# Optimization experiments

Measured on AMD Instinct MI355X. Metric: run time of the kernel, lower is better.

The kernel has to match this reference:

```python
import jax, jax.numpy as jnp
import numpy as np

NUM_HEADS = 16
EPS = 1e-15


def setup_inputs() -> dict:
    key = jax.random.key(0)
    k1, k2, k3, k4 = jax.random.split(key, 4)
    B, N, C = 4, 16384, 512
    x = jax.random.normal(k1, (B, N, C), dtype=jnp.float32)
    qkv_weight = jax.random.normal(k2, (3 * C, C), dtype=jnp.float32) * 0.02
    proj_weight = jax.random.normal(k3, (C, C), dtype=jnp.float32) * 0.02
    proj_bias = jax.random.normal(k4, (C,), dtype=jnp.float32) * 0.02
    return {"x": x, "qkv_weight": qkv_weight, "proj_weight": proj_weight, "proj_bias": proj_bias}


def reference(x, qkv_weight, proj_weight, proj_bias):
    B, N, C = x.shape
    H = NUM_HEADS
    D = C // H
    # fused linear + ReLU on q,k (v stays linear, per backward: grad_v has no relu mask)
    qkv = (x @ qkv_weight.T).reshape(B, N, 3, C)
    q = jax.nn.relu(qkv[:, :, 0]).reshape(B, N, H, D)
    k = jax.nn.relu(qkv[:, :, 1]).reshape(B, N, H, D)
    v = qkv[:, :, 2].reshape(B, N, H, D)
    qf = q.astype(jnp.float32)
    kf = k.astype(jnp.float32)
    vf = v.astype(jnp.float32)
    # pad v with a ones column -> normalizer row in vk (pad_vk_mm_fwd)
    v_pad = jnp.concatenate([vf, jnp.ones_like(vf[..., :1])], axis=-1)  # [B,N,H,D+1]
    vk = jnp.einsum('bnhc,bnhd->bhcd', v_pad, kf)  # [B,H,D+1,D] accumulated in fp32
    vk_q = jnp.einsum('bnhd,bhcd->bnhc', qf, vk)  # [B,N,H,D+1]
    # fused division by normalizer (vk_q_mm_divide_fwd)
    proj_input = (vk_q[..., :-1] / (vk_q[..., -1:] + EPS)).astype(x.dtype).reshape(B, N, C)
    return proj_input @ proj_weight.T + proj_bias
```

## Files before the change

kernel.cpp:

```cpp
#include <hip/hip_runtime.h>
#include <stdint.h>

#define NB 4
#define SEQ 16384
#define CH 512
#define NH 16
#define HD 32
#define QKVC 1536
#define MROWS (NB * SEQ)

typedef unsigned short u16;
typedef __attribute__((ext_vector_type(8))) short bf16x8;
typedef __attribute__((ext_vector_type(4))) float f32x4;

__device__ __forceinline__ float bf2f(u16 u) {
  union { unsigned int i; float f; } c; c.i = ((unsigned int)u) << 16; return c.f;
}
__device__ __forceinline__ u16 f2bf(float f) {
  union { float f; unsigned int i; } c; c.f = f;
  return (u16)((c.i + 0x7fffu + ((c.i >> 16) & 1u)) >> 16);
}

__device__ __forceinline__ void async16(const u16* g, u16* l) {
  __builtin_amdgcn_global_load_lds((const __attribute__((address_space(1))) void*)g,
                                   (__attribute__((address_space(3))) void*)l,
                                   16, 0, 0);
}

__global__ void prep_kernel(const float* __restrict__ x,
                            const float* __restrict__ qw,
                            const float* __restrict__ pw,
                            u16* __restrict__ xb,
                            u16* __restrict__ qwb,
                            u16* __restrict__ pwb,
                            float* __restrict__ vk) {
  int gid = blockIdx.x * blockDim.x + threadIdx.x;
  int stride = gridDim.x * blockDim.x;

  const float4* x4 = (const float4*)x;
  ushort4* xb4 = (ushort4*)xb;
  for (int i = gid; i < (MROWS * CH / 4); i += stride) {
    float4 v = x4[i];
    ushort4 o; o.x = f2bf(v.x); o.y = f2bf(v.y); o.z = f2bf(v.z); o.w = f2bf(v.w);
    xb4[i] = o;
  }
  const float4* q4 = (const float4*)qw;
  ushort4* qwb4 = (ushort4*)qwb;
  for (int i = gid; i < (QKVC * CH / 4); i += stride) {
    float4 v = q4[i];
    ushort4 o; o.x = f2bf(v.x); o.y = f2bf(v.y); o.z = f2bf(v.z); o.w = f2bf(v.w);
    qwb4[i] = o;
  }
  const float4* p4 = (const float4*)pw;
  ushort4* pwb4 = (ushort4*)pwb;
  for (int i = gid; i < (CH * CH / 4); i += stride) {
    float4 v = p4[i];
    ushort4 o; o.x = f2bf(v.x); o.y = f2bf(v.y); o.z = f2bf(v.z); o.w = f2bf(v.w);
    pwb4[i] = o;
  }
  float4 z; z.x = 0.f; z.y = 0.f; z.z = 0.f; z.w = 0.f;
  float4* vk4 = (float4*)vk;
  for (int i = gid; i < (NB * NH * 33 * 32 / 4); i += stride) vk4[i] = z;
}

template <int N_DIM, bool RELU_QK, bool FINAL>
__global__ __launch_bounds__(256) void gemm_bt_kernel(
    const u16* __restrict__ A, const u16* __restrict__ Bm,
    void* __restrict__ Out, const float* __restrict__ bias) {
  constexpr int K = 512;
  __shared__ u16 As[128 * 32];
  __shared__ u16 Bs[128 * 32];

  const int tid = threadIdx.x;
  const int lane = tid & 63;
  const int w = tid >> 6;
  const long row0 = (long)blockIdx.y * 128;
  const int col0 = blockIdx.x * 128;

  const int l4r = lane >> 2;
  const int l4c = (lane & 3) * 8;
  const int wr = w >> 1, wc = w & 1;
  const int fr = lane & 15;
  const int koff = (lane >> 4) * 8;

  f32x4 acc[4][4];
#pragma unroll
  for (int m = 0; m < 4; m++)
#pragma unroll
    for (int n = 0; n < 4; n++) {
      f32x4 z = {0.f, 0.f, 0.f, 0.f};
      acc[m][n] = z;
    }

  for (int k0 = 0; k0 < K; k0 += 32) {
#pragma unroll
    for (int i = 0; i < 2; i++) {
      const int r = w * 32 + i * 16;
      async16(A + (row0 + r + l4r) * K + k0 + l4c, &As[r * 32]);
      async16(Bm + (long)(col0 + r + l4r) * K + k0 + l4c, &Bs[r * 32]);
    }
    __syncthreads();
    bf16x8 af[4], bfr[4];
#pragma unroll
    for (int m = 0; m < 4; m++)
      af[m] = *(const bf16x8*)&As[(wr * 64 + m * 16 + fr) * 32 + koff];
#pragma unroll
    for (int n = 0; n < 4; n++)
      bfr[n] = *(const bf16x8*)&Bs[(wc * 64 + n * 16 + fr) * 32 + koff];
#pragma unroll
    for (int m = 0; m < 4; m++)
#pragma unroll
      for (int n = 0; n < 4; n++)
        acc[m][n] = __builtin_amdgcn_mfma_f32_16x16x32_bf16(af[m], bfr[n], acc[m][n], 0, 0, 0);
    __syncthreads();
  }

  const long rbase = row0 + wr * 64;
  const int cbase = col0 + wc * 64;
#pragma unroll
  for (int m = 0; m < 4; m++)
#pragma unroll
    for (int n = 0; n < 4; n++)
#pragma unroll
      for (int j = 0; j < 4; j++) {
        long gr = rbase + m * 16 + (lane >> 4) * 4 + j;
        int gc = cbase + n * 16 + fr;
        float v = acc[m][n][j];
        if constexpr (FINAL) {
          ((float*)Out)[gr * N_DIM + gc] = v + bias[gc];
        } else {
          if (RELU_QK && gc < 1024) v = fmaxf(v, 0.f);
          ((u16*)Out)[gr * N_DIM + gc] = f2bf(v);
        }
      }
}

__global__ __launch_bounds__(256) void vk_kernel(const u16* __restrict__ qkv,
                                                 float* __restrict__ vk) {
  __shared__ u16 tile[4][64 * 64];
  __shared__ float red[1056];

  const int tid = threadIdx.x;
  const int lane = tid & 63;
  const int w = tid >> 6;

  for (int i = tid; i < 1056; i += 256) red[i] = 0.f;
  __syncthreads();

  const int bh = blockIdx.x >> 4;
  const int split = blockIdx.x & 15;
  const int b = bh >> 4, h = bh & 15;

  const int s = lane & 7;
  const int rl = lane >> 3;
  const size_t gbase = (size_t)b * SEQ * QKVC + 512 + (size_t)(s >> 2) * 512 +
                       h * 32 + (s & 3) * 8;

  f32x4 acc[2][2];
  f32x4 accs[2];
#pragma unroll
  for (int tc = 0; tc < 2; tc++) {
    f32x4 z = {0.f, 0.f, 0.f, 0.f};
    accs[tc] = z;
#pragma unroll
    for (int td = 0; td < 2; td++) acc[tc][td] = z;
  }
  bf16x8 ones;
#pragma unroll
  for (int j = 0; j < 8; j++) ones[j] = (short)0x3F80;

  const int m = lane & 15;
  const int g = lane >> 4;
  u16* tw = tile[w];
  const int n0w = split * 1024 + w * 256;

  for (int t = 0; t < 4; ++t) {
    const int nt = n0w + t * 64;
#pragma unroll
    for (int p = 0; p < 8; ++p)
      async16(qkv + gbase + (size_t)(nt + p * 8 + rl) * QKVC, &tw[p * 512]);
    asm volatile("s_waitcnt vmcnt(0)" ::: "memory");
#pragma unroll
    for (int kk = 0; kk < 2; ++kk) {
      bf16x8 av[2], bk[2];
#pragma unroll
      for (int tc = 0; tc < 2; tc++)
#pragma unroll
        for (int j = 0; j < 8; j++)
          av[tc][j] = (short)tw[(kk * 32 + g * 8 + j) * 64 + 32 + tc * 16 + m];
#pragma unroll
      for (int td = 0; td < 2; td++)
#pragma unroll
        for (int j = 0; j < 8; j++)
          bk[td][j] = (short)tw[(kk * 32 + g * 8 + j) * 64 + td * 16 + m];
#pragma unroll
      for (int tc = 0; tc < 2; tc++)
#pragma unroll
        for (int td = 0; td < 2; td++)
          acc[tc][td] = __builtin_amdgcn_mfma_f32_16x16x32_bf16(av[tc], bk[td], acc[tc][td], 0, 0, 0);
#pragma unroll
      for (int td = 0; td < 2; td++)
        accs[td] = __builtin_amdgcn_mfma_f32_16x16x32_bf16(ones, bk[td], accs[td], 0, 0, 0);
    }
  }

#pragma unroll
  for (int tc = 0; tc < 2; tc++)
#pragma unroll
    for (int td = 0; td < 2; td++)
#pragma unroll
      for (int j = 0; j < 4; j++)
        atomicAdd(&red[(tc * 16 + g * 4 + j) * 32 + td * 16 + m], acc[tc][td][j]);
  if (lane < 16) {
#pragma unroll
    for (int td = 0; td < 2; td++)
      atomicAdd(&red[1024 + td * 16 + lane], accs[td][0]);
  }
  __syncthreads();
  float* dst = vk + (size_t)bh * 1056;
  for (int i = tid; i < 1056; i += 256) atomicAdd(&dst[i], red[i]);
}

__global__ __launch_bounds__(256) void vkq_kernel(const u16* __restrict__ qkv,
                                                  const float* __restrict__ vk,
                                                  u16* __restrict__ pi) {
  __shared__ float vkl[8 * 1056];
  __shared__ u16 ob[32 * 256];

  const int tid = threadIdx.x;
  const int chunk = blockIdx.x & 511;
  const int hh = (blockIdx.x >> 9) & 1;
  const int b = blockIdx.x >> 10;
  const int n0 = chunk * 32;

  const float* vg = vk + (size_t)(b * NH + hh * 8) * 1056;
  for (int i = tid; i < 8 * 1056; i += 256) vkl[i] = vg[i];
  __syncthreads();

  const int nl = tid & 31;
  const int hl = tid >> 5;
  const float* vkh = &vkl[hl * 1056];

  const u16* qp = qkv + ((size_t)b * SEQ + n0 + nl) * QKVC + (hh * 8 + hl) * 32;
  float qf[32];
#pragma unroll
  for (int s2 = 0; s2 < 4; ++s2) {
    bf16x8 qv = *(const bf16x8*)(qp + s2 * 8);
#pragma unroll
    for (int j = 0; j < 8; ++j) qf[s2 * 8 + j] = bf2f((u16)qv[j]);
  }

  float num[32];
#pragma unroll
  for (int c = 0; c < 32; ++c) {
    float a = 0.f;
#pragma unroll
    for (int d4 = 0; d4 < 8; ++d4) {
      f32x4 vv = *(const f32x4*)&vkh[c * 32 + d4 * 4];
      a = fmaf(qf[d4 * 4 + 0], vv[0], a);
      a = fmaf(qf[d4 * 4 + 1], vv[1], a);
      a = fmaf(qf[d4 * 4 + 2], vv[2], a);
      a = fmaf(qf[d4 * 4 + 3], vv[3], a);
    }
    num[c] = a;
  }
  float den = 0.f;
#pragma unroll
  for (int d4 = 0; d4 < 8; ++d4) {
    f32x4 vv = *(const f32x4*)&vkh[32 * 32 + d4 * 4];
    den = fmaf(qf[d4 * 4 + 0], vv[0], den);
    den = fmaf(qf[d4 * 4 + 1], vv[1], den);
    den = fmaf(qf[d4 * 4 + 2], vv[2], den);
    den = fmaf(qf[d4 * 4 + 3], vv[3], den);
  }
  const float r = 1.0f / (den + 1e-15f);
#pragma unroll
  for (int c = 0; c < 32; ++c) ob[nl * 256 + hl * 32 + c] = f2bf(num[c] * r);
  __syncthreads();

  u16* pg = pi + ((size_t)b * SEQ + n0) * CH + hh * 256;
  for (int i = tid; i < 1024; i += 256) {
    const int n = i >> 5;
    const int u = i & 31;
    *(bf16x8*)(pg + (size_t)n * CH + u * 8) = *(const bf16x8*)&ob[i * 8];
  }
}

extern "C" void kernel_launch(void* const* d_in, const int* in_sizes, int n_in,
                              void* d_out, int out_size, void* d_ws, size_t ws_size,
                              hipStream_t stream) {
  const float* x = (const float*)d_in[0];
  const float* qw = (const float*)d_in[1];
  const float* pw = (const float*)d_in[2];
  const float* bias = (const float*)d_in[3];

  char* ws = (char*)d_ws;
  u16* qkv = (u16*)(ws);
  u16* xb = (u16*)(ws + 201326592);
  u16* qwb = (u16*)(ws + 268435456);
  u16* pwb = (u16*)(ws + 270008320);
  float* vk = (float*)(ws + 270532608);
  u16* pi = xb;

  prep_kernel<<<2048, 256, 0, stream>>>(x, qw, pw, xb, qwb, pwb, vk);
  gemm_bt_kernel<QKVC, true, false>
      <<<dim3(QKVC / 128, MROWS / 128), 256, 0, stream>>>(xb, qwb, qkv, nullptr);
  vk_kernel<<<NB * NH * 16, 256, 0, stream>>>(qkv, vk);
  vkq_kernel<<<NB * 2 * (SEQ / 32), 256, 0, stream>>>(qkv, vk, pi);
  gemm_bt_kernel<CH, false, true>
      <<<dim3(CH / 128, MROWS / 128), 256, 0, stream>>>(pi, pwb, d_out, bias);
}
```

Measured before the change: 360.8 us.

## Replace GEMM with 256x256-tile 8-wave pipelined kernel using swizzled LDS

Both GEMMs move from a 128x128 tile with 4 waves and a single-buffered K=32 loop to a 256x256 tile with 8 waves. The new loop uses K=64 steps with double-buffered async global-to-LDS loads staged in halves, XOR-swizzled LDS addressing to avoid bank conflicts, and s_setprio around MFMA bursts. A remapped block index groups workgroups for better L2 locality. The goal is more data reuse per load and overlap of memory traffic with MFMA work. In exchange it uses 128KB of LDS and more registers, and its manual waitcnt and barrier scheduling is fragile.

Measured after the change: 319.4 us. 11.5% less time.

```diff
diff --git a/kernel.cpp b/kernel.cpp
--- a/kernel.cpp
+++ b/kernel.cpp
@@ -64,67 +64,161 @@
 }
 
 template <int N_DIM, bool RELU_QK, bool FINAL>
-__global__ __launch_bounds__(256) void gemm_bt_kernel(
+__global__ __launch_bounds__(512, 2) void gemm8p_kernel(
     const u16* __restrict__ A, const u16* __restrict__ Bm,
     void* __restrict__ Out, const float* __restrict__ bias) {
-  constexpr int K = 512;
-  __shared__ u16 As[128 * 32];
-  __shared__ u16 Bs[128 * 32];
+  __shared__ __align__(16) u16 lds[65536];
 
   const int tid = threadIdx.x;
   const int lane = tid & 63;
   const int w = tid >> 6;
-  const long row0 = (long)blockIdx.y * 128;
-  const int col0 = blockIdx.x * 128;
-
-  const int l4r = lane >> 2;
-  const int l4c = (lane & 3) * 8;
-  const int wr = w >> 1, wc = w & 1;
+  const int wr = w >> 2;
+  const int wc = w & 3;
   const int fr = lane & 15;
-  const int koff = (lane >> 4) * 8;
-
-  f32x4 acc[4][4];
-#pragma unroll
-  for (int m = 0; m < 4; m++)
+  const int g = lane >> 4;
+  const int xr = (fr & 7) << 3;
+
+  const int gridX = N_DIM / 256;
+  const int nwg = gridX * (MROWS / 256);
+  int bid = blockIdx.y * gridX + blockIdx.x;
+  bid = (bid & 7) * (nwg >> 3) + (bid >> 3);
+  const long row0 = (long)(bid / gridX) * 256;
+  const long col0 = (long)(bid % gridX) * 256;
+
+  const int trow = tid >> 3;
+  const int tcol = ((tid & 7) * 8) ^ (((tid >> 3) & 7) << 3);
+
+#define STAGE_A(kt_, h_)                                                      \
+  do {                                                                        \
+    u16* lb_ = &lds[(((kt_) & 1) * 2 + (h_)) * 8192 + w * 512];               \
+    const u16* ga_ = A + (size_t)(row0 + (h_) * 128 + trow) * 512 +           \
+                     (kt_) * 64 + tcol;                                       \
+    async16(ga_, lb_);                                                        \
+    async16(ga_ + 64 * 512, lb_ + 4096);                                      \
+  } while (0)
+
+#define STAGE_B(kt_, h_)                                                      \
+  do {                                                                        \
+    u16* lb_ = &lds[32768 + (((kt_) & 1) * 2 + (h_)) * 8192 + w * 512];       \
+    const u16* gb_ = Bm + (size_t)(col0 + (h_) * 128 + trow) * 512 +          \
+                     (kt_) * 64 + tcol;                                       \
+    async16(gb_, lb_);                                                        \
+    async16(gb_ + 64 * 512, lb_ + 4096);                                      \
+  } while (0)
+
+  f32x4 acc[8][4];
+#pragma unroll
+  for (int m = 0; m < 8; m++)
 #pragma unroll
     for (int n = 0; n < 4; n++) {
       f32x4 z = {0.f, 0.f, 0.f, 0.f};
       acc[m][n] = z;
     }
-
-  for (int k0 = 0; k0 < K; k0 += 32) {
-#pragma unroll
-    for (int i = 0; i < 2; i++) {
-      const int r = w * 32 + i * 16;
-      async16(A + (row0 + r + l4r) * K + k0 + l4c, &As[r * 32]);
-      async16(Bm + (long)(col0 + r + l4r) * K + k0 + l4c, &Bs[r * 32]);
+  bf16x8 a[4][2], b[4][2];
+
+  STAGE_B(0, 0); STAGE_A(0, 0); STAGE_B(0, 1); STAGE_A(0, 1);
+  STAGE_B(1, 0); STAGE_A(1, 0);
+  asm volatile("s_waitcnt vmcnt(4)" ::: "memory");
+  __builtin_amdgcn_s_barrier();
+
+#pragma unroll
+  for (int kt = 0; kt < 8; ++kt) {
+    const int abase = ((kt & 1) * 2 + wr) * 8192;
+    const int bbase = 32768 + ((kt & 1) * 2 + (wc >> 1)) * 8192 + (wc & 1) * 4096;
+
+#pragma unroll
+    for (int m = 0; m < 4; ++m)
+#pragma unroll
+      for (int kk = 0; kk < 2; ++kk)
+        a[m][kk] = *(const bf16x8*)&lds[abase + (m * 16 + fr) * 64 + ((kk * 32 + g * 8) ^ xr)];
+#pragma unroll
+    for (int n = 0; n < 2; ++n)
+#pragma unroll
+      for (int kk = 0; kk < 2; ++kk)
+        b[n][kk] = *(const bf16x8*)&lds[bbase + (n * 16 + fr) * 64 + ((kk * 32 + g * 8) ^ xr)];
+    if (kt < 7) STAGE_B(kt + 1, 1);
+    __builtin_amdgcn_s_barrier();
+    asm volatile("s_waitcnt lgkmcnt(0)" ::: "memory");
+    __builtin_amdgcn_s_setprio(1);
+#pragma unroll
+    for (int m = 0; m < 4; ++m)
+#pragma unroll
+      for (int n = 0; n < 2; ++n)
+#pragma unroll
+        for (int kk = 0; kk < 2; ++kk)
+          acc[m][n] = __builtin_amdgcn_mfma_f32_16x16x32_bf16(a[m][kk], b[n][kk], acc[m][n], 0, 0, 0);
+    __builtin_amdgcn_s_setprio(0);
+    __builtin_amdgcn_s_barrier();
+
+#pragma unroll
+    for (int n = 0; n < 2; ++n)
+#pragma unroll
+      for (int kk = 0; kk < 2; ++kk)
+        b[2 + n][kk] = *(const bf16x8*)&lds[bbase + ((n + 2) * 16 + fr) * 64 + ((kk * 32 + g * 8) ^ xr)];
+    if (kt < 7) STAGE_A(kt + 1, 1);
+    __builtin_amdgcn_s_barrier();
+    asm volatile("s_waitcnt lgkmcnt(0)" ::: "memory");
+    __builtin_amdgcn_s_setprio(1);
+#pragma unroll
+    for (int m = 0; m < 4; ++m)
+#pragma unroll
+      for (int n = 0; n < 2; ++n)
+#pragma unroll
+        for (int kk = 0; kk < 2; ++kk)
+          acc[m][2 + n] = __builtin_amdgcn_mfma_f32_16x16x32_bf16(a[m][kk], b[2 + n][kk], acc[m][2 + n], 0, 0, 0);
+    __builtin_amdgcn_s_setprio(0);
+    __builtin_amdgcn_s_barrier();
+
+#pragma unroll
+    for (int m = 0; m < 4; ++m)
+#pragma unroll
+      for (int kk = 0; kk < 2; ++kk)
+        a[m][kk] = *(const bf16x8*)&lds[abase + ((m + 4) * 16 + fr) * 64 + ((kk * 32 + g * 8) ^ xr)];
+    if (kt < 6) STAGE_B(kt + 2, 0);
+    __builtin_amdgcn_s_barrier();
+    asm volatile("s_waitcnt lgkmcnt(0)" ::: "memory");
+    __builtin_amdgcn_s_setprio(1);
+#pragma unroll
+    for (int m = 0; m < 4; ++m)
+#pragma unroll
+      for (int n = 0; n < 2; ++n)
+#pragma unroll
+        for (int kk = 0; kk < 2; ++kk)
+          acc[4 + m][2 + n] = __builtin_amdgcn_mfma_f32_16x16x32_bf16(a[m][kk], b[2 + n][kk], acc[4 + m][2 + n], 0, 0, 0);
+    __builtin_amdgcn_s_setprio(0);
+    __builtin_amdgcn_s_barrier();
+
+    if (kt < 6) {
+      STAGE_A(kt + 2, 0);
+      asm volatile("s_waitcnt vmcnt(4)" ::: "memory");
+    } else {
+      asm volatile("s_waitcnt vmcnt(0)" ::: "memory");
     }
-    __syncthreads();
-    bf16x8 af[4], bfr[4];
-#pragma unroll
-    for (int m = 0; m < 4; m++)
-      af[m] = *(const bf16x8*)&As[(wr * 64 + m * 16 + fr) * 32 + koff];
-#pragma unroll
-    for (int n = 0; n < 4; n++)
-      bfr[n] = *(const bf16x8*)&Bs[(wc * 64 + n * 16 + fr) * 32 + koff];
-#pragma unroll
-    for (int m = 0; m < 4; m++)
-#pragma unroll
-      for (int n = 0; n < 4; n++)
-        acc[m][n] = __builtin_amdgcn_mfma_f32_16x16x32_bf16(af[m], bfr[n], acc[m][n], 0, 0, 0);
-    __syncthreads();
-  }
-
-  const long rbase = row0 + wr * 64;
-  const int cbase = col0 + wc * 64;
-#pragma unroll
-  for (int m = 0; m < 4; m++)
-#pragma unroll
-    for (int n = 0; n < 4; n++)
-#pragma unroll
-      for (int j = 0; j < 4; j++) {
-        long gr = rbase + m * 16 + (lane >> 4) * 4 + j;
-        int gc = cbase + n * 16 + fr;
+    __builtin_amdgcn_s_barrier();
+    __builtin_amdgcn_s_setprio(1);
+#pragma unroll
+    for (int m = 0; m < 4; ++m)
+#pragma unroll
+      for (int n = 0; n < 2; ++n)
+#pragma unroll
+        for (int kk = 0; kk < 2; ++kk)
+          acc[4 + m][n] = __builtin_amdgcn_mfma_f32_16x16x32_bf16(a[m][kk], b[n][kk], acc[4 + m][n], 0, 0, 0);
+    __builtin_amdgcn_s_setprio(0);
+    __builtin_amdgcn_s_barrier();
+  }
+#undef STAGE_A
+#undef STAGE_B
+
+  const long rbase = row0 + wr * 128;
+  const long cbase = col0 + wc * 64;
+#pragma unroll
+  for (int m = 0; m < 8; ++m)
+#pragma unroll
+    for (int n = 0; n < 4; ++n)
+#pragma unroll
+      for (int j = 0; j < 4; ++j) {
+        long gr = rbase + m * 16 + g * 4 + j;
+        long gc = cbase + n * 16 + fr;
         float v = acc[m][n][j];
         if constexpr (FINAL) {
           ((float*)Out)[gr * N_DIM + gc] = v + bias[gc];
@@ -303,10 +397,10 @@
   u16* pi = xb;
 
   prep_kernel<<<2048, 256, 0, stream>>>(x, qw, pw, xb, qwb, pwb, vk);
-  gemm_bt_kernel<QKVC, true, false>
-      <<<dim3(QKVC / 128, MROWS / 128), 256, 0, stream>>>(xb, qwb, qkv, nullptr);
+  gemm8p_kernel<QKVC, true, false>
+      <<<dim3(QKVC / 256, MROWS / 256), 512, 0, stream>>>(xb, qwb, qkv, nullptr);
   vk_kernel<<<NB * NH * 16, 256, 0, stream>>>(qkv, vk);
   vkq_kernel<<<NB * 2 * (SEQ / 32), 256, 0, stream>>>(qkv, vk, pi);
-  gemm_bt_kernel<CH, false, true>
-      <<<dim3(CH / 128, MROWS / 128), 256, 0, stream>>>(pi, pwb, d_out, bias);
-}
+  gemm8p_kernel<CH, false, true>
+      <<<dim3(CH / 256, MROWS / 256), 512, 0, stream>>>(pi, pwb, d_out, bias);
+}
```
